# Kernel tuning notes

Hardware: AMD Instinct MI355X
Metric: run time of the kernel (lower is better)

Reference implementation:

```python
import jax, jax.numpy as jnp
import numpy as np

N_HEADS = 12

def setup_inputs() -> dict:
    key = jax.random.key(0)
    k1, k2, k3 = jax.random.split(key, 3)
    B, L, D = 2, 2048, 768
    x = jax.random.normal(k1, (B, L, D), dtype=jnp.float32)
    attention_mask = jnp.ones((B, L), dtype=jnp.int32)  # 1 = real token
    w_qkv = jax.random.normal(k2, (D, 3 * D), dtype=jnp.float32) * (1.0 / np.sqrt(D))
    b_qkv = jnp.zeros((3 * D,), dtype=jnp.float32)
    w_out = jax.random.normal(k3, (D, D), dtype=jnp.float32) * (1.0 / np.sqrt(D))
    b_out = jnp.zeros((D,), dtype=jnp.float32)
    return {"x": x, "attention_mask": attention_mask, "w_qkv": w_qkv,
            "b_qkv": b_qkv, "w_out": w_out, "b_out": b_out}

def reference(x, attention_mask, w_qkv, b_qkv, w_out, b_out):
    B, L, D = x.shape
    H = N_HEADS
    dk = D // H
    # fused QKV projection
    qkv = jnp.einsum('bld,de->ble', x, w_qkv) + b_qkv  # (B,L,3D)
    q, k, v = jnp.split(qkv, 3, axis=-1)
    def to_heads(t):
        return t.reshape(B, L, H, dk).transpose(0, 2, 1, 3)  # (B,H,L,dk)
    q, k, v = to_heads(q), to_heads(k), to_heads(v)
    scale = 1.0 / jnp.sqrt(jnp.asarray(dk, dtype=x.dtype))
    scores = jnp.einsum('bhqd,bhkd->bhqk', q, k) * scale  # (B,H,L,L)
    mask = (attention_mask != 0)[:, None, None, :]  # (B,1,1,L), True = keep
    neg = jnp.asarray(jnp.finfo(scores.dtype).min, dtype=scores.dtype)
    scores = jnp.where(mask, scores, neg)
    weights = jax.nn.softmax(scores, axis=-1)
    out = jnp.einsum('bhqk,bhkd->bhqd', weights, v)  # (B,H,L,dk)
    out = out.transpose(0, 2, 1, 3).reshape(B, L, D)
    return jnp.einsum('bld,de->ble', out, w_out) + b_out
```

## Files before the change

kernel.cpp:

```cpp
#include <hip/hip_runtime.h>

typedef __bf16 bf16;
typedef bf16 bf16x4 __attribute__((ext_vector_type(4)));
typedef bf16 bf16x8 __attribute__((ext_vector_type(8)));
typedef float f32x4 __attribute__((ext_vector_type(4)));

#define MFMA16(A, B, C) __builtin_amdgcn_mfma_f32_16x16x32_bf16(A, B, C, 0, 0, 0)
#define NEG_BIG -30000.0f

#define GLOAD_LDS16(gptr, lptr)                                                \
    __builtin_amdgcn_global_load_lds(                                          \
        (__attribute__((address_space(1))) void*)(gptr),                       \
        (__attribute__((address_space(3))) void*)(lptr), 16, 0, 0)

#define SW(r, c8) ((r) * 64 + (((((c8) >> 3) ^ ((r) & 7))) << 3))

__global__ void mark_k(float* __restrict__ out, float val, int n) {
    int i = blockIdx.x * 256 + threadIdx.x;
    if (i < n) out[i] = val;
}

__global__ __launch_bounds__(256) void cvt_x_k(const float* __restrict__ src,
                                               bf16* __restrict__ dst, int n) {
    int i = (blockIdx.x * 256 + threadIdx.x) * 8;
    if (i >= n) return;
    float4 a = *(const float4*)&src[i];
    float4 b = *(const float4*)&src[i + 4];
    bf16x8 w;
    w[0] = (bf16)a.x; w[1] = (bf16)a.y; w[2] = (bf16)a.z; w[3] = (bf16)a.w;
    w[4] = (bf16)b.x; w[5] = (bf16)b.y; w[6] = (bf16)b.z; w[7] = (bf16)b.w;
    *(bf16x8*)&dst[i] = w;
}

__global__ __launch_bounds__(256) void transpose_cvt_tiled(
    const float* __restrict__ src, bf16* __restrict__ dst, int R, int C) {
    __shared__ float t[32][33];
    int tid = threadIdx.x, tx = tid & 31, ty = tid >> 5;
    int bx = blockIdx.x * 32, by = blockIdx.y * 32;
#pragma unroll
    for (int i = 0; i < 4; ++i) {
        int row = by + ty + i * 8;
        t[ty + i * 8][tx] = src[(size_t)row * C + bx + tx];
    }
    __syncthreads();
#pragma unroll
    for (int i = 0; i < 4; ++i) {
        int outrow = bx + ty + i * 8;
        dst[(size_t)outrow * R + by + tx] = (bf16)t[tx][ty + i * 8];
    }
}

#define CLD 136

__global__ __launch_bounds__(256) void gemm_qkv_v4(
    const bf16* __restrict__ A, const bf16* __restrict__ B,
    const float* __restrict__ bias, bf16* __restrict__ Qh,
    bf16* __restrict__ Kh, bf16* __restrict__ Vth) {
    __shared__ __align__(16) bf16 SMEM[128 * CLD];
    bf16* As = SMEM;
    bf16* Bs = SMEM + 8192;

    int tid = threadIdx.x, lane = tid & 63, wave = tid >> 6;
    int quad = lane >> 4, l16 = lane & 15;
    int wr = wave >> 1, wc = wave & 1;
    int m0 = blockIdx.y * 128, n0 = blockIdx.x * 128;
    const int K = 768;
    const f32x4 fz = {0.f, 0.f, 0.f, 0.f};
    f32x4 acc[4][4];
#pragma unroll
    for (int nj = 0; nj < 4; ++nj)
#pragma unroll
        for (int mi = 0; mi < 4; ++mi) acc[nj][mi] = fz;
    const bf16* Ablk = A + (size_t)m0 * K;
    const bf16* Bblk = B + (size_t)n0 * K;
    int lrow8 = lane >> 3;
    int sc = ((lane & 7) ^ (lrow8 & 7)) << 3;

    for (int k0 = 0; k0 < K; k0 += 64) {
        __syncthreads();
#pragma unroll
        for (int i = 0; i < 4; ++i) {
            int r0 = i * 32 + wave * 8;
            int row = r0 + lrow8;
            GLOAD_LDS16(&Ablk[(size_t)row * K + k0 + sc], &As[r0 * 64]);
            GLOAD_LDS16(&Bblk[(size_t)row * K + k0 + sc], &Bs[r0 * 64]);
        }
        __syncthreads();
        bf16x8 af[2][4], bfv[2][4];
#pragma unroll
        for (int t = 0; t < 4; ++t)
#pragma unroll
            for (int hh = 0; hh < 2; ++hh) {
                af[hh][t]  = *(const bf16x8*)&As[SW(wr * 64 + t * 16 + l16, hh * 32 + quad * 8)];
                bfv[hh][t] = *(const bf16x8*)&Bs[SW(wc * 64 + t * 16 + l16, hh * 32 + quad * 8)];
            }
#pragma unroll
        for (int nj = 0; nj < 4; ++nj)
#pragma unroll
            for (int mi = 0; mi < 4; ++mi) {
                acc[nj][mi] = MFMA16(bfv[0][nj], af[0][mi], acc[nj][mi]);
                acc[nj][mi] = MFMA16(bfv[1][nj], af[1][mi], acc[nj][mi]);
            }
    }

    int which = n0 / 768;
    int h0 = (n0 % 768) >> 6;
    int b = m0 >> 11, l0 = m0 & 2047;
    __syncthreads();

    if (which == 2) {
#pragma unroll
        for (int nj = 0; nj < 4; ++nj) {
            int cl0 = wc * 64 + nj * 16 + quad * 4;
            float4 bv4 = *(const float4*)&bias[n0 + cl0];
            float bv[4] = {bv4.x, bv4.y, bv4.z, bv4.w};
#pragma unroll
            for (int mi = 0; mi < 4; ++mi) {
                int xrl = wr * 64 + mi * 16 + l16;
#pragma unroll
                for (int r = 0; r < 4; ++r)
                    SMEM[(cl0 + r) * CLD + xrl] = (bf16)(acc[nj][mi][r] + bv[r]);
            }
        }
    } else {
        float s = (which == 0) ? 0.125f : 1.0f;
#pragma unroll
        for (int nj = 0; nj < 4; ++nj) {
            int cl0 = wc * 64 + nj * 16 + quad * 4;
            float4 bv4 = *(const float4*)&bias[n0 + cl0];
            float bv[4] = {bv4.x, bv4.y, bv4.z, bv4.w};
#pragma unroll
            for (int mi = 0; mi < 4; ++mi) {
                int xrl = wr * 64 + mi * 16 + l16;
                bf16x4 v;
#pragma unroll
                for (int r = 0; r < 4; ++r) v[r] = (bf16)((acc[nj][mi][r] + bv[r]) * s);
                *(bf16x4*)&SMEM[xrl * CLD + cl0] = v;
            }
        }
    }
    __syncthreads();

    if (which == 2) {
#pragma unroll
        for (int i = 0; i < 8; ++i) {
            int idx = i * 256 + tid;
            int cl = idx >> 4, ch = idx & 15;
            int d = cl & 63, h = h0 + (cl >> 6);
            bf16x8 v = *(const bf16x8*)&SMEM[cl * CLD + ch * 8];
            *(bf16x8*)&Vth[((size_t)(b * 12 + h) * 64 + d) * 2048 + l0 + ch * 8] = v;
        }
    } else {
        bf16* dst = (which == 0) ? Qh : Kh;
#pragma unroll
        for (int i = 0; i < 8; ++i) {
            int idx = i * 256 + tid;
            int rr = idx >> 4, ch = idx & 15;
            int h = h0 + (ch >> 3), d0 = (ch & 7) * 8;
            bf16x8 v = *(const bf16x8*)&SMEM[rr * CLD + ch * 8];
            *(bf16x8*)&dst[((size_t)(b * 12 + h) * 2048 + l0 + rr) * 64 + d0] = v;
        }
    }
}

__global__ __launch_bounds__(128) void gemm_out_v3(
    const bf16* __restrict__ A, const bf16* __restrict__ B,
    const float* __restrict__ bias, float* __restrict__ C) {
    __shared__ __align__(16) bf16 As[128 * 32];
    __shared__ __align__(16) bf16 Bs[64 * 32];
    int tid = threadIdx.x, lane = tid & 63, wave = tid >> 6;
    int quad = lane >> 4, l16 = lane & 15;
    int m0 = blockIdx.y * 128, n0 = blockIdx.x * 64;
    const int K = 768, N = 768;
    const f32x4 fz = {0.f, 0.f, 0.f, 0.f};
    f32x4 acc[4][4];
#pragma unroll
    for (int mi = 0; mi < 4; ++mi)
#pragma unroll
        for (int nj = 0; nj < 4; ++nj) acc[mi][nj] = fz;
    const bf16* Ablk = A + (size_t)m0 * K;
    const bf16* Bblk = B + (size_t)n0 * K;
    int grow = tid >> 2, gcol = (tid & 3) * 8;

    for (int k0 = 0; k0 < K; k0 += 32) {
        __syncthreads();
#pragma unroll
        for (int i = 0; i < 4; ++i)
            GLOAD_LDS16(&Ablk[(size_t)(i * 32 + grow) * K + k0 + gcol],
                        &As[i * 1024 + wave * 512]);
#pragma unroll
        for (int i = 0; i < 2; ++i)
            GLOAD_LDS16(&Bblk[(size_t)(i * 32 + grow) * K + k0 + gcol],
                        &Bs[i * 1024 + wave * 512]);
        __syncthreads();
        bf16x8 af[4], bfv[4];
#pragma unroll
        for (int t = 0; t < 4; ++t) {
            af[t]  = *(const bf16x8*)&As[(wave * 64 + t * 16 + l16) * 32 + quad * 8];
            bfv[t] = *(const bf16x8*)&Bs[(t * 16 + l16) * 32 + quad * 8];
        }
#pragma unroll
        for (int mi = 0; mi < 4; ++mi)
#pragma unroll
            for (int nj = 0; nj < 4; ++nj)
                acc[mi][nj] = MFMA16(af[mi], bfv[nj], acc[mi][nj]);
    }

#pragma unroll
    for (int nj = 0; nj < 4; ++nj) {
        int col = n0 + nj * 16 + l16;
        float bv = bias[col];
#pragma unroll
        for (int mi = 0; mi < 4; ++mi)
#pragma unroll
            for (int r = 0; r < 4; ++r) {
                int row = m0 + wave * 64 + mi * 16 + quad * 4 + r;
                C[(size_t)row * N + col] = acc[mi][nj][r] + bv;
            }
    }
}

#define PLD 72

__global__ __launch_bounds__(256) void flash_attn(
    const bf16* __restrict__ Q, const bf16* __restrict__ K,
    const bf16* __restrict__ V, const int* __restrict__ mask,
    bf16* __restrict__ ctx) {
    __shared__ __align__(16) bf16 Ks[2][64 * 64];
    __shared__ __align__(16) bf16 Vs[2][64 * 64];
    __shared__ __align__(16) bf16 Ps[4][16 * PLD];
    __shared__ float maskS[2048];
    __shared__ int cleanF;

    int tid = threadIdx.x, lane = tid & 63, wave = tid >> 6;
    int quad = lane >> 4, l16 = lane & 15;
    int bh = blockIdx.y, b = bh / 12;
    int q0 = blockIdx.x * 128 + wave * 32;

    bf16x8 aq[2][2];
#pragma unroll
    for (int qt = 0; qt < 2; ++qt) {
        const bf16* Qp = Q + ((size_t)bh * 2048 + q0 + qt * 16 + l16) * 64;
        aq[qt][0] = *(const bf16x8*)(Qp + quad * 8);
        aq[qt][1] = *(const bf16x8*)(Qp + 32 + quad * 8);
    }

    if (tid == 0) cleanF = 1;
    __syncthreads();
    const int* mrow = mask + b * 2048;
    int myclean = 1;
#pragma unroll
    for (int i = 0; i < 8; ++i) {
        int idx = i * 256 + tid;
        int mv = mrow[idx];
        maskS[idx] = mv ? 0.0f : NEG_BIG;
        myclean &= (mv != 0);
    }
    if (!myclean) cleanF = 0;

    const f32x4 fz = {0.f, 0.f, 0.f, 0.f};
    f32x4 o[2][4];
    float m_i[2], l_i[2];
#pragma unroll
    for (int qt = 0; qt < 2; ++qt) {
        m_i[qt] = NEG_BIG; l_i[qt] = 0.f;
#pragma unroll
        for (int dt = 0; dt < 4; ++dt) o[qt][dt] = fz;
    }

    int srow = tid >> 3;
    int sc8  = (tid & 7) * 8;
    const bf16* Kbase = K + (size_t)bh * 2048 * 64;
    const bf16* Vbase = V + (size_t)bh * 64 * 2048;

#pragma unroll
    for (int i = 0; i < 2; ++i) {
        int row = srow + i * 32;
        *(bf16x8*)&Ks[0][SW(row, sc8)] =
            *(const bf16x8*)&Kbase[(size_t)row * 64 + sc8];
        *(bf16x8*)&Vs[0][SW(row, sc8)] =
            *(const bf16x8*)&Vbase[(size_t)row * 2048 + sc8];
    }
    __syncthreads();
    int clean = cleanF;

    int p = 0;
    for (int kb = 0; kb < 2048; kb += 64) {
        __syncthreads();

        if (kb + 64 < 2048) {
            int nb = kb + 64;
#pragma unroll
            for (int i = 0; i < 2; ++i) {
                int row = srow + i * 32;
                *(bf16x8*)&Ks[1 - p][SW(row, sc8)] =
                    *(const bf16x8*)&Kbase[(size_t)(nb + row) * 64 + sc8];
                *(bf16x8*)&Vs[1 - p][SW(row, sc8)] =
                    *(const bf16x8*)&Vbase[(size_t)row * 2048 + nb + sc8];
            }
        }

        f32x4 s[2][4];
#pragma unroll
        for (int ct = 0; ct < 4; ++ct) {
            int krow = ct * 16 + l16;
            bf16x8 kf0 = *(const bf16x8*)&Ks[p][SW(krow, quad * 8)];
            bf16x8 kf1 = *(const bf16x8*)&Ks[p][SW(krow, 32 + quad * 8)];
#pragma unroll
            for (int qt = 0; qt < 2; ++qt) {
                f32x4 t = fz;
                t = MFMA16(kf0, aq[qt][0], t);
                t = MFMA16(kf1, aq[qt][1], t);
                s[qt][ct] = t;
            }
        }

        if (!clean) {
#pragma unroll
            for (int ct = 0; ct < 4; ++ct) {
                const float* mk = &maskS[kb + ct * 16 + quad * 4];
                float4 mv = *(const float4*)mk;
                float ma[4] = {mv.x, mv.y, mv.z, mv.w};
#pragma unroll
                for (int qt = 0; qt < 2; ++qt)
#pragma unroll
                    for (int r = 0; r < 4; ++r) s[qt][ct][r] += ma[r];
            }
        }

        float alpha[2];
#pragma unroll
        for (int qt = 0; qt < 2; ++qt) {
            float mx = NEG_BIG;
#pragma unroll
            for (int ct = 0; ct < 4; ++ct)
#pragma unroll
                for (int r = 0; r < 4; ++r) mx = fmaxf(mx, s[qt][ct][r]);
            mx = fmaxf(mx, __shfl_xor(mx, 16));
            mx = fmaxf(mx, __shfl_xor(mx, 32));
            float nm = fmaxf(m_i[qt], mx);
            alpha[qt] = __expf(m_i[qt] - nm);
            m_i[qt] = nm;
            float sum = 0.f;
#pragma unroll
            for (int ct = 0; ct < 4; ++ct)
#pragma unroll
                for (int r = 0; r < 4; ++r) {
                    float pv = __expf(s[qt][ct][r] - nm);
                    s[qt][ct][r] = pv;
                    sum += pv;
                }
            sum += __shfl_xor(sum, 16);
            sum += __shfl_xor(sum, 32);
            l_i[qt] = l_i[qt] * alpha[qt] + sum;
        }

#pragma unroll
        for (int qt = 0; qt < 2; ++qt) {
            float ab[4];
#pragma unroll
            for (int r = 0; r < 4; ++r)
                ab[r] = __shfl(alpha[qt], (lane & 48) | (quad * 4 + r));
#pragma unroll
            for (int dt = 0; dt < 4; ++dt)
#pragma unroll
                for (int r = 0; r < 4; ++r) o[qt][dt][r] *= ab[r];
        }

        bf16x8 vf[2][4];
#pragma unroll
        for (int ks = 0; ks < 2; ++ks)
#pragma unroll
            for (int dt = 0; dt < 4; ++dt)
                vf[ks][dt] = *(const bf16x8*)&Vs[p][SW(dt * 16 + l16, ks * 32 + quad * 8)];

#pragma unroll
        for (int qt = 0; qt < 2; ++qt) {
#pragma unroll
            for (int ct = 0; ct < 4; ++ct) {
                bf16x4 pk;
#pragma unroll
                for (int r = 0; r < 4; ++r) pk[r] = (bf16)s[qt][ct][r];
                *(bf16x4*)&Ps[wave][l16 * PLD + ct * 16 + quad * 4] = pk;
            }
#pragma unroll
            for (int ks = 0; ks < 2; ++ks) {
                bf16x8 ap = *(const bf16x8*)&Ps[wave][l16 * PLD + ks * 32 + quad * 8];
#pragma unroll
                for (int dt = 0; dt < 4; ++dt)
                    o[qt][dt] = MFMA16(ap, vf[ks][dt], o[qt][dt]);
            }
        }
        p ^= 1;
    }

    int h = bh % 12;
#pragma unroll
    for (int qt = 0; qt < 2; ++qt) {
        float linv[4];
#pragma unroll
        for (int r = 0; r < 4; ++r)
            linv[r] = 1.0f / __shfl(l_i[qt], (lane & 48) | (quad * 4 + r));
#pragma unroll
        for (int dt = 0; dt < 4; ++dt)
#pragma unroll
            for (int r = 0; r < 4; ++r) {
                int qrow = q0 + qt * 16 + quad * 4 + r;
                ctx[((size_t)b * 2048 + qrow) * 768 + h * 64 + dt * 16 + l16] =
                    (bf16)(o[qt][dt][r] * linv[r]);
            }
    }
}

extern "C" void kernel_launch(void* const* d_in, const int* in_sizes, int n_in,
                              void* d_out, int out_size, void* d_ws, size_t ws_size,
                              hipStream_t stream) {
    float* out = (float*)d_out;

    const float* x = nullptr; const int* mask = nullptr;
    const float* w_qkv = nullptr; const float* b_qkv = nullptr;
    const float* w_out = nullptr; const float* b_out = nullptr;
    int found = 0;
    for (int i = 0; i < n_in; ++i) {
        switch (in_sizes[i]) {
            case 3145728: x     = (const float*)d_in[i]; found |= 1;  break;
            case 4096:    mask  = (const int*)  d_in[i]; found |= 2;  break;
            case 1769472: w_qkv = (const float*)d_in[i]; found |= 4;  break;
            case 2304:    b_qkv = (const float*)d_in[i]; found |= 8;  break;
            case 589824:  w_out = (const float*)d_in[i]; found |= 16; break;
            case 768:     b_out = (const float*)d_in[i]; found |= 32; break;
        }
    }
    if (found != 63) {
        mark_k<<<(out_size + 255) / 256, 256, 0, stream>>>(
            out, 200.0f + (float)found, out_size);
        return;
    }

    const int M = 4096, D = 768, N3 = 2304;
    const size_t HEADS_ELEMS = (size_t)24 * 2048 * 64;

    bf16* ws    = (bf16*)d_ws;
    bf16* Kh    = ws;
    bf16* Vth   = Kh + HEADS_ELEMS;
    bf16* ctx   = Vth + HEADS_ELEMS;
    bf16* wqkvT = ctx + (size_t)M * D;
    bf16* woutT = wqkvT + (size_t)N3 * D;
    bf16* Qh    = (bf16*)d_out;
    bf16* xb    = (bf16*)d_out + HEADS_ELEMS;

    cvt_x_k<<<(M * D / 8 + 255) / 256, 256, 0, stream>>>(x, xb, M * D);
    transpose_cvt_tiled<<<dim3(2304 / 32, 768 / 32), 256, 0, stream>>>(
        w_qkv, wqkvT, 768, 2304);
    transpose_cvt_tiled<<<dim3(768 / 32, 768 / 32), 256, 0, stream>>>(
        w_out, woutT, 768, 768);

    gemm_qkv_v4<<<dim3(N3 / 128, M / 128), 256, 0, stream>>>(
        xb, wqkvT, b_qkv, Qh, Kh, Vth);

    flash_attn<<<dim3(2048 / 128, 24), 256, 0, stream>>>(Qh, Kh, Vth, mask, ctx);

    gemm_out_v3<<<dim3(D / 64, M / 128), 128, 0, stream>>>(
        ctx, woutT, b_out, out);
}
```

Before: 202.1 us.

## Double-buffer LDS tiles in QKV and output GEMMs with XOR swizzle

After: 200.6 us. Within noise of the previous version (-0.7%).

```diff
diff --git a/kernel.cpp b/kernel.cpp
--- a/kernel.cpp
+++ b/kernel.cpp
@@ -14,6 +14,7 @@
         (__attribute__((address_space(3))) void*)(lptr), 16, 0, 0)
 
 #define SW(r, c8) ((r) * 64 + (((((c8) >> 3) ^ ((r) & 7))) << 3))
+#define SW32(r, q) ((r) * 32 + ((((q) ^ ((r) & 3))) << 3))
 
 __global__ void mark_k(float* __restrict__ out, float val, int n) {
     int i = blockIdx.x * 256 + threadIdx.x;
@@ -52,14 +53,11 @@
 
 #define CLD 136
 
-__global__ __launch_bounds__(256) void gemm_qkv_v4(
+__global__ __launch_bounds__(256) void gemm_qkv_v5(
     const bf16* __restrict__ A, const bf16* __restrict__ B,
     const float* __restrict__ bias, bf16* __restrict__ Qh,
     bf16* __restrict__ Kh, bf16* __restrict__ Vth) {
     __shared__ __align__(16) bf16 SMEM[128 * CLD];
-    bf16* As = SMEM;
-    bf16* Bs = SMEM + 8192;
-
     int tid = threadIdx.x, lane = tid & 63, wave = tid >> 6;
     int quad = lane >> 4, l16 = lane & 15;
     int wr = wave >> 1, wc = wave & 1;
@@ -73,34 +71,51 @@
         for (int mi = 0; mi < 4; ++mi) acc[nj][mi] = fz;
     const bf16* Ablk = A + (size_t)m0 * K;
     const bf16* Bblk = B + (size_t)n0 * K;
-    int lrow8 = lane >> 3;
-    int sc = ((lane & 7) ^ (lrow8 & 7)) << 3;
-
-    for (int k0 = 0; k0 < K; k0 += 64) {
+
+    int srow = lane >> 2;
+    int c    = lane & 3;
+
+#pragma unroll
+    for (int i = 0; i < 2; ++i) {
+        int r0 = i * 64 + wave * 16;
+        int row = r0 + srow;
+        int sc = (c ^ (row & 3)) << 3;
+        GLOAD_LDS16(&Ablk[(size_t)row * K + sc], &SMEM[r0 * 32]);
+        GLOAD_LDS16(&Bblk[(size_t)row * K + sc], &SMEM[4096 + r0 * 32]);
+    }
+
+    int p = 0;
+    for (int k0 = 0; k0 < K; k0 += 32) {
         __syncthreads();
-#pragma unroll
-        for (int i = 0; i < 4; ++i) {
-            int r0 = i * 32 + wave * 8;
-            int row = r0 + lrow8;
-            GLOAD_LDS16(&Ablk[(size_t)row * K + k0 + sc], &As[r0 * 64]);
-            GLOAD_LDS16(&Bblk[(size_t)row * K + k0 + sc], &Bs[r0 * 64]);
-        }
-        __syncthreads();
-        bf16x8 af[2][4], bfv[2][4];
-#pragma unroll
-        for (int t = 0; t < 4; ++t)
-#pragma unroll
-            for (int hh = 0; hh < 2; ++hh) {
-                af[hh][t]  = *(const bf16x8*)&As[SW(wr * 64 + t * 16 + l16, hh * 32 + quad * 8)];
-                bfv[hh][t] = *(const bf16x8*)&Bs[SW(wc * 64 + t * 16 + l16, hh * 32 + quad * 8)];
-            }
+
+        if (k0 + 32 < K) {
+            int kn = k0 + 32;
+#pragma unroll
+            for (int i = 0; i < 2; ++i) {
+                int r0 = i * 64 + wave * 16;
+                int row = r0 + srow;
+                int sc = (c ^ (row & 3)) << 3;
+                GLOAD_LDS16(&Ablk[(size_t)row * K + kn + sc],
+                            &SMEM[(1 - p) * 8192 + r0 * 32]);
+                GLOAD_LDS16(&Bblk[(size_t)row * K + kn + sc],
+                            &SMEM[4096 + (1 - p) * 8192 + r0 * 32]);
+            }
+        }
+
+        const bf16* Asp = &SMEM[p * 8192];
+        const bf16* Bsp = &SMEM[4096 + p * 8192];
+        bf16x8 af[4], bfv[4];
+#pragma unroll
+        for (int t = 0; t < 4; ++t) {
+            af[t]  = *(const bf16x8*)&Asp[SW32(wr * 64 + t * 16 + l16, quad)];
+            bfv[t] = *(const bf16x8*)&Bsp[SW32(wc * 64 + t * 16 + l16, quad)];
+        }
 #pragma unroll
         for (int nj = 0; nj < 4; ++nj)
 #pragma unroll
-            for (int mi = 0; mi < 4; ++mi) {
-                acc[nj][mi] = MFMA16(bfv[0][nj], af[0][mi], acc[nj][mi]);
-                acc[nj][mi] = MFMA16(bfv[1][nj], af[1][mi], acc[nj][mi]);
-            }
+            for (int mi = 0; mi < 4; ++mi)
+                acc[nj][mi] = MFMA16(bfv[nj], af[mi], acc[nj][mi]);
+        p ^= 1;
     }
 
     int which = n0 / 768;
@@ -163,11 +178,11 @@
     }
 }
 
-__global__ __launch_bounds__(128) void gemm_out_v3(
+__global__ __launch_bounds__(128) void gemm_out_v4(
     const bf16* __restrict__ A, const bf16* __restrict__ B,
     const float* __restrict__ bias, float* __restrict__ C) {
-    __shared__ __align__(16) bf16 As[128 * 32];
-    __shared__ __align__(16) bf16 Bs[64 * 32];
+    __shared__ __align__(16) bf16 As[2][128 * 32];
+    __shared__ __align__(16) bf16 Bs[2][64 * 32];
     int tid = threadIdx.x, lane = tid & 63, wave = tid >> 6;
     int quad = lane >> 4, l16 = lane & 15;
     int m0 = blockIdx.y * 128, n0 = blockIdx.x * 64;
@@ -180,30 +195,57 @@
         for (int nj = 0; nj < 4; ++nj) acc[mi][nj] = fz;
     const bf16* Ablk = A + (size_t)m0 * K;
     const bf16* Bblk = B + (size_t)n0 * K;
-    int grow = tid >> 2, gcol = (tid & 3) * 8;
-
+    int srow = lane >> 2, c = lane & 3;
+
+#pragma unroll
+    for (int i = 0; i < 4; ++i) {
+        int r0 = i * 32 + wave * 16;
+        int row = r0 + srow;
+        int sc = (c ^ (row & 3)) << 3;
+        GLOAD_LDS16(&Ablk[(size_t)row * K + sc], &As[0][r0 * 32]);
+    }
+#pragma unroll
+    for (int i = 0; i < 2; ++i) {
+        int r0 = i * 32 + wave * 16;
+        int row = r0 + srow;
+        int sc = (c ^ (row & 3)) << 3;
+        GLOAD_LDS16(&Bblk[(size_t)row * K + sc], &Bs[0][r0 * 32]);
+    }
+
+    int p = 0;
     for (int k0 = 0; k0 < K; k0 += 32) {
         __syncthreads();
-#pragma unroll
-        for (int i = 0; i < 4; ++i)
-            GLOAD_LDS16(&Ablk[(size_t)(i * 32 + grow) * K + k0 + gcol],
-                        &As[i * 1024 + wave * 512]);
-#pragma unroll
-        for (int i = 0; i < 2; ++i)
-            GLOAD_LDS16(&Bblk[(size_t)(i * 32 + grow) * K + k0 + gcol],
-                        &Bs[i * 1024 + wave * 512]);
-        __syncthreads();
+
+        if (k0 + 32 < K) {
+            int kn = k0 + 32;
+#pragma unroll
+            for (int i = 0; i < 4; ++i) {
+                int r0 = i * 32 + wave * 16;
+                int row = r0 + srow;
+                int sc = (c ^ (row & 3)) << 3;
+                GLOAD_LDS16(&Ablk[(size_t)row * K + kn + sc], &As[1 - p][r0 * 32]);
+            }
+#pragma unroll
+            for (int i = 0; i < 2; ++i) {
+                int r0 = i * 32 + wave * 16;
+                int row = r0 + srow;
+                int sc = (c ^ (row & 3)) << 3;
+                GLOAD_LDS16(&Bblk[(size_t)row * K + kn + sc], &Bs[1 - p][r0 * 32]);
+            }
+        }
+
         bf16x8 af[4], bfv[4];
 #pragma unroll
         for (int t = 0; t < 4; ++t) {
-            af[t]  = *(const bf16x8*)&As[(wave * 64 + t * 16 + l16) * 32 + quad * 8];
-            bfv[t] = *(const bf16x8*)&Bs[(t * 16 + l16) * 32 + quad * 8];
+            af[t]  = *(const bf16x8*)&As[p][SW32(wave * 64 + t * 16 + l16, quad)];
+            bfv[t] = *(const bf16x8*)&Bs[p][SW32(t * 16 + l16, quad)];
         }
 #pragma unroll
         for (int mi = 0; mi < 4; ++mi)
 #pragma unroll
             for (int nj = 0; nj < 4; ++nj)
                 acc[mi][nj] = MFMA16(af[mi], bfv[nj], acc[mi][nj]);
+        p ^= 1;
     }
 
 #pragma unroll
@@ -455,11 +497,11 @@
     transpose_cvt_tiled<<<dim3(768 / 32, 768 / 32), 256, 0, stream>>>(
         w_out, woutT, 768, 768);
 
-    gemm_qkv_v4<<<dim3(N3 / 128, M / 128), 256, 0, stream>>>(
+    gemm_qkv_v5<<<dim3(N3 / 128, M / 128), 256, 0, stream>>>(
         xb, wqkvT, b_qkv, Qh, Kh, Vth);
 
     flash_attn<<<dim3(2048 / 128, 24), 256, 0, stream>>>(Qh, Kh, Vth, mask, ctx);
 
-    gemm_out_v3<<<dim3(D / 64, M / 128), 128, 0, stream>>>(
+    gemm_out_v4<<<dim3(D / 64, M / 128), 128, 0, stream>>>(
         ctx, woutT, b_out, out);
 }
```
